# Performance work log

Hardware: AMD Instinct MI355X
Metric: run time of the kernel (lower is better)

## Reference

```python
import jax, jax.numpy as jnp
import numpy as np

N = 4096
DIN, DOUT, HID, CUTS = 16, 16, 16, 8
RADIUS = 9.0
SCALES = (1.0, 2.0, 3.0, 5.0, 10.0)
REG = 0.01
CHUNK = 512
GROUPS = 4
DINF = DIN + 2 * len(SCALES)  # 26


def leaky(v):
    return jnp.where(v >= 0, v, 0.2 * v)


def sqdist(a, b):
    d2 = jnp.sum(a * a, -1)[:, None] + jnp.sum(b * b, -1)[None, :] - 2.0 * (a @ b.T)
    return jnp.maximum(d2, 0.0)


def tangent_vectors(n):
    # Duff et al. branchless orthonormal basis, as in dMaSIF geometry_processing
    x, y, z = n[..., 0], n[..., 1], n[..., 2]
    s = jnp.where(z >= 0, 1.0, -1.0)
    a = -1.0 / (s + z)
    b = x * y * a
    t1 = jnp.stack([1.0 + s * x * x * a, s * b, -s * x], -1)
    t2 = jnp.stack([b, s + y * y * a, -y], -1)
    return jnp.stack([t1, t2], axis=-2)  # (..., 2, 3)


def group_norm(x, w, b, eps=1e-5):
    # torch GroupNorm(4, C) applied on (1, C, N): normalize over (C/G, N) per group
    n, c = x.shape
    xt = x.T.reshape(GROUPS, c // GROUPS, n)
    m = jnp.mean(xt, axis=(1, 2), keepdims=True)
    v = jnp.mean((xt - m) ** 2, axis=(1, 2), keepdims=True)
    xt = (xt - m) / jnp.sqrt(v + eps)
    return (xt.reshape(c, n) * w[:, None] + b[:, None]).T


def curvature_features(verts, normals):
    # dMaSIF curvatures(): per-scale Gaussian-window covariances, shape operator S = PPt^-1 PQt
    # Pairwise sums factorized into matmuls with the (N,N) window (no (N,N,8) intermediates).
    n_pts = verts.shape[0]
    d2 = sqdist(verts, verts)
    xx = (verts[:, :, None] * verts[:, None, :]).reshape(n_pts, 9)
    feats = []
    for s in SCALES:
        w = jnp.exp(-d2 / (2.0 * s * s))
        u_n = w @ normals  # scale-smoothed normals
        ns = u_n / jnp.maximum(jnp.linalg.norm(u_n, axis=-1, keepdims=True), 1e-12)
        uv = tangent_vectors(ns)  # (N,2,3)
        s0 = jnp.sum(w, 1)
        sx = w @ verts
        sn = w @ ns
        sxx = (w @ xx).reshape(n_pts, 3, 3)
        xn = (verts[:, :, None] * ns[:, None, :]).reshape(n_pts, 9)
        sxn = (w @ xn).reshape(n_pts, 3, 3)
        # sum_j w_ij (x_j-x_i)(x_j-x_i)^T  and  sum_j w_ij (x_j-x_i)(n_j-n_i)^T
        cxx = sxx - verts[:, :, None] * sx[:, None, :] - sx[:, :, None] * verts[:, None, :] \
              + s0[:, None, None] * verts[:, :, None] * verts[:, None, :]
        cxn = sxn - verts[:, :, None] * sn[:, None, :] - sx[:, :, None] * ns[:, None, :] \
              + s0[:, None, None] * verts[:, :, None] * ns[:, None, :]
        ppt = jnp.einsum('nka,nab,nlb->nkl', uv, cxx, uv) + REG * jnp.eye(2, dtype=verts.dtype)
        pqt = jnp.einsum('nka,nab,nlb->nkl', uv, cxn, uv)
        S = jnp.linalg.solve(ppt, pqt)  # (N,2,2)
        feats.append(jnp.clip(S[:, 0, 0] + S[:, 1, 1], -1.0, 1.0))            # mean curvature
        feats.append(jnp.clip(S[:, 0, 0] * S[:, 1, 1] - S[:, 0, 1] * S[:, 1, 0], -1.0, 1.0))  # gauss
    return jnp.stack(feats, -1)  # (N, 2*len(SCALES))


def _forward(verts, vnormals, x, os_w1, os_b1, os_w2, os_b2,
             ni_w1, ni_b1, ni_w2, ni_b2, gn_in_w, gn_in_b,
             cv_a1, cv_b1, cv_a2, cv_b2, no_w1, no_b1, no_w2, no_b2,
             gn_out_w, gn_out_b, ll_w1, ll_b1, ll_w2, ll_b2, lt_w, lt_b):
    curv = curvature_features(verts, vnormals)
    xf = jnp.concatenate([x, curv], axis=-1)  # (N, DINF)
    w = leaky(xf @ os_w1.T + os_b1) @ os_w2.T + os_b2  # orientation scores (N,1)

    # --- load_mesh: steer tangent frames along the gradient of w ---
    p = verts / RADIUS
    ndot = vnormals @ vnormals.T
    W = jnp.exp(-sqdist(p, p) * (2.0 - ndot) ** 2)  # pseudo-geodesic Gaussian window
    uv = tangent_vectors(vnormals)  # (N,2,3)
    ov3 = W @ (w * p) - (W @ w) * p  # sum_j W_ij w_j (x_j - x_i), factorized
    ov = jnp.einsum('nkd,nd->nk', uv, ov3) + 1e-5
    u = ov / jnp.sqrt(jnp.sum(ov * ov, -1, keepdims=True))
    ex, ey = u[:, 0:1], u[:, 1:2]
    u0, v0 = uv[:, 0], uv[:, 1]
    nuv = jnp.concatenate([vnormals[:, None, :],
                           (ex * u0 + ey * v0)[:, None, :],
                           (-ey * u0 + ex * v0)[:, None, :]], axis=1)  # (N,3,3)

    # --- dMaSIFConv layer ---
    h = leaky(leaky(xf @ ni_w1.T + ni_b1) @ ni_w2.T + ni_b2)
    h = group_norm(h, gn_in_w, gn_in_b)  # (N, HID)
    n_all = nuv[:, 0]
    nc = N // CHUNK
    pc = p.reshape(nc, CHUNK, 3)
    nuvc = nuv.reshape(nc, CHUNK, 3, 3)

    def block(args):
        pi, nuvi = args  # (C,3), (C,3,3)
        dx = p[None, :, :] - pi[:, None, :]  # (C,N,3)
        d2 = jnp.sum(dx * dx, -1)
        win = jnp.exp(-d2 * (2.0 - nuvi[:, 0] @ n_all.T) ** 2)  # (C,N)
        X = jnp.einsum('ckd,cnd->cnk', nuvi, dx)  # local coords (C,N,3)
        y = jax.nn.relu(X @ cv_a1.T + cv_b1) @ cv_a2.T + cv_b2  # filter MLP (C,N,HID)
        return jnp.einsum('cn,cnh,nh->ch', win, y, h)

    xi = jax.lax.map(jax.checkpoint(block), (pc, nuvc)).reshape(N, HID)
    xi = group_norm(leaky(leaky(xi @ no_w1.T + no_b1) @ no_w2.T + no_b2), gn_out_w, gn_out_b)
    xi = jax.nn.relu(xi @ ll_w1.T + ll_b1) @ ll_w2.T + ll_b2  # linear_layers[0]
    return xf @ lt_w.T + lt_b + xi  # linear_transform skip + conv branch


def setup_inputs():
    key = jax.random.key(0)
    ks = jax.random.split(key, 20)

    def lin(k, o, i):
        wk = jax.random.fold_in(k, 0)
        bk = jax.random.fold_in(k, 1)
        return ((1.0 / np.sqrt(i)) * jax.random.normal(wk, (o, i)),
                0.01 * jax.random.normal(bk, (o,)))

    verts = 10.0 * jax.random.normal(ks[0], (N, 3))
    vn = jax.random.normal(ks[1], (N, 3))
    vnormals = vn / jnp.linalg.norm(vn, axis=-1, keepdims=True)
    x = jax.random.normal(ks[2], (N, DIN))
    os_w1, os_b1 = lin(ks[3], DOUT, DINF)
    os_w2, os_b2 = lin(ks[4], 1, DOUT)
    ni_w1, ni_b1 = lin(ks[5], HID, DINF)
    ni_w2, ni_b2 = lin(ks[6], HID, HID)
    cv_a1 = jax.random.normal(ks[7], (CUTS, 3))
    cv_b1 = jax.random.uniform(ks[8], (CUTS,)) * 0.8 * jnp.sqrt(jnp.sum(cv_a1 ** 2, -1))
    cv_a2 = jax.random.uniform(ks[9], (HID, CUTS), minval=-1.0, maxval=1.0) / np.sqrt(CUTS)
    cv_b2 = jax.random.normal(ks[10], (HID,)) * 0.5 * jnp.sqrt(jnp.sum(cv_a2 ** 2, -1))
    no_w1, no_b1 = lin(ks[11], DOUT, HID)
    no_w2, no_b2 = lin(ks[12], DOUT, DOUT)
    ll_w1, ll_b1 = lin(ks[13], DOUT, DOUT)
    ll_w2, ll_b2 = lin(ks[14], DOUT, DOUT)
    lt_w, lt_b = lin(ks[15], DOUT, DINF)
    return {'verts': verts, 'vnormals': vnormals, 'x': x,
            'os_w1': os_w1, 'os_b1': os_b1, 'os_w2': os_w2, 'os_b2': os_b2,
            'ni_w1': ni_w1, 'ni_b1': ni_b1, 'ni_w2': ni_w2, 'ni_b2': ni_b2,
            'gn_in_w': jnp.ones(HID), 'gn_in_b': jnp.zeros(HID),
            'cv_a1': cv_a1, 'cv_b1': cv_b1, 'cv_a2': cv_a2, 'cv_b2': cv_b2,
            'no_w1': no_w1, 'no_b1': no_b1, 'no_w2': no_w2, 'no_b2': no_b2,
            'gn_out_w': jnp.ones(DOUT), 'gn_out_b': jnp.zeros(DOUT),
            'll_w1': ll_w1, 'll_b1': ll_b1, 'll_w2': ll_w2, 'll_b2': ll_b2,
            'lt_w': lt_w, 'lt_b': lt_b}


def reference(verts, vnormals, x, os_w1, os_b1, os_w2, os_b2,
              ni_w1, ni_b1, ni_w2, ni_b2, gn_in_w, gn_in_b,
              cv_a1, cv_b1, cv_a2, cv_b2, no_w1, no_b1, no_w2, no_b2,
              gn_out_w, gn_out_b, ll_w1, ll_b1, ll_w2, ll_b2, lt_w, lt_b):
    return _forward(verts, vnormals, x, os_w1, os_b1, os_w2, os_b2,
                    ni_w1, ni_b1, ni_w2, ni_b2, gn_in_w, gn_in_b,
                    cv_a1, cv_b1, cv_a2, cv_b2, no_w1, no_b1, no_w2, no_b2,
                    gn_out_w, gn_out_b, ll_w1, ll_b1, ll_w2, ll_b2, lt_w, lt_b)
```

## Files before the change

### kernel.cpp

```cpp
#include <hip/hip_runtime.h>
#include <hip/hip_bf16.h>
#include <math.h>

#define NPTS 4096
#define DINF 26
#define LOG2E 1.44269504088896f

typedef float f32x4v __attribute__((ext_vector_type(4)));
typedef __bf16 bf16x8v __attribute__((ext_vector_type(8)));

__device__ __forceinline__ float ldb(const float* p, int i){ return p[i]; }
__device__ __forceinline__ float lk(float v){ return v >= 0.0f ? v : 0.2f*v; }
__device__ __forceinline__ float wsum64(float v){
#pragma unroll
  for(int o=32;o>0;o>>=1) v += __shfl_down(v,o);
  return v;
}
__device__ __forceinline__ unsigned short f2bf(float f){
  return __builtin_bit_cast(unsigned short, __float2bfloat16(f));
}
__device__ __forceinline__ float bf2f(unsigned short u){
  return __bfloat162float(__builtin_bit_cast(__hip_bfloat16, u));
}
__device__ __forceinline__ unsigned pk2(float a, float b){
  return (unsigned)f2bf(a) | ((unsigned)f2bf(b)<<16);
}
__device__ __forceinline__ void split2(float a, float b, unsigned& h, unsigned& l){
  unsigned short ah=f2bf(a), bh=f2bf(b);
  float ar = a - bf2f(ah), br = b - bf2f(bh);
  h = (unsigned)ah | ((unsigned)bh<<16);
  l = (unsigned)f2bf(ar) | ((unsigned)f2bf(br)<<16);
}
__device__ __forceinline__ void wave_lds_fence(){
  __builtin_amdgcn_wave_barrier();
  __builtin_amdgcn_s_waitcnt(0xC07F);
  __builtin_amdgcn_wave_barrier();
}
__device__ __forceinline__ void tangent(float nx,float ny,float nz,float* t1,float* t2){
  float s = (nz >= 0.0f) ? 1.0f : -1.0f;
  float a = -1.0f/(s+nz);
  float b = nx*ny*a;
  t1[0]=1.0f+s*nx*nx*a; t1[1]=s*b; t1[2]=-s*nx;
  t2[0]=b; t2[1]=s+ny*ny*a; t2[2]=-ny;
}

__global__ __launch_bounds__(256) void k0_convert(const float* __restrict__ verts,
                                                  const float* __restrict__ vnorm,
                                                  const float* __restrict__ x,
                                                  float* __restrict__ vertsF,
                                                  float* __restrict__ nF,
                                                  float* __restrict__ pF,
                                                  float* __restrict__ xfF){
  int i = blockIdx.x*blockDim.x + threadIdx.x;
  if(i >= NPTS) return;
#pragma unroll
  for(int d=0;d<3;d++){
    float v = verts[i*3+d];
    vertsF[i*3+d]=v;
    pF[i*3+d]=v*(1.0f/9.0f);
    nF[i*3+d]=vnorm[i*3+d];
  }
#pragma unroll
  for(int c=0;c<16;c++) xfF[i*DINF+c]=x[i*16+c];
}

__global__ __launch_bounds__(512) void k1m(const float* __restrict__ vertsF,
                                           const float* __restrict__ nF,
                                           float* __restrict__ sc){
  __shared__ unsigned short fbh[8][64][18];
  __shared__ unsigned short fbl[8][64][18];
  __shared__ float vq[8][64][4];
  __shared__ float red[8][16][16];
  const float c2e[5] = {0.5f*LOG2E, 0.125f*LOG2E, (1.0f/18.0f)*LOG2E,
                        0.02f*LOG2E, 0.005f*LOG2E};
  int lane = threadIdx.x & 63, w = threadIdx.x >> 6;
  int c16 = lane & 15, q = lane >> 4;
  int i0 = blockIdx.x*16;
  int ia = i0 + c16;
  float vix=vertsF[ia*3+0], viy=vertsF[ia*3+1], viz=vertsF[ia*3+2];
  float nsqi = vix*vix+viy*viy+viz*viz;
  f32x4v acc[5];
#pragma unroll
  for(int s=0;s<5;s++) acc[s] = (f32x4v){0.0f,0.0f,0.0f,0.0f};

#pragma unroll 1
  for(int jb = w*512; jb < (w+1)*512; jb += 64){
    int j = jb + lane;
    float vx=vertsF[j*3+0], vy=vertsF[j*3+1], vz=vertsF[j*3+2];
    float nx=nF[j*3+0], ny=nF[j*3+1], nz=nF[j*3+2];
    float nsq = vx*vx+vy*vy+vz*vz;
    unsigned* fh = (unsigned*)&fbh[w][lane][0];
    unsigned* fl = (unsigned*)&fbl[w][lane][0];
    unsigned h,l;
    split2(1.0f, vx, h,l);      fh[0]=h; fl[0]=l;
    split2(vy, vz, h,l);        fh[1]=h; fl[1]=l;
    split2(vx*vx, vx*vy, h,l);  fh[2]=h; fl[2]=l;
    split2(vx*vz, vy*vy, h,l);  fh[3]=h; fl[3]=l;
    split2(vy*vz, vz*vz, h,l);  fh[4]=h; fl[4]=l;
    split2(nx, ny, h,l);        fh[5]=h; fl[5]=l;
    split2(nz, 0.0f, h,l);      fh[6]=h; fl[6]=l;
    fh[7]=0u; fl[7]=0u; fh[8]=0u; fl[8]=0u;
    *(float4*)&vq[w][lane][0] = make_float4(vx,vy,vz,nsq);
    wave_lds_fence();
#pragma unroll
    for(int q2=0;q2<2;q2++){
      int rb = q2*32 + q*8;
      bf16x8v bh, bl;
#pragma unroll
      for(int t=0;t<8;t++){
        bh[t] = __builtin_bit_cast(__bf16, fbh[w][rb+t][c16]);
        bl[t] = __builtin_bit_cast(__bf16, fbl[w][rb+t][c16]);
      }
      bf16x8v af[5];
#pragma unroll
      for(int t=0;t<8;t++){
        float4 vv = *(const float4*)&vq[w][rb+t][0];
        float dot = vix*vv.x + viy*vv.y + viz*vv.z;
        float d2 = fmaxf(nsqi + vv.w - 2.0f*dot, 0.0f);
#pragma unroll
        for(int s=0;s<5;s++)
          af[s][t] = __builtin_bit_cast(__bf16, f2bf(exp2f(-d2*c2e[s])));
      }
#pragma unroll
      for(int s=0;s<5;s++){
        acc[s] = __builtin_amdgcn_mfma_f32_16x16x32_bf16(af[s], bh, acc[s], 0,0,0);
        acc[s] = __builtin_amdgcn_mfma_f32_16x16x32_bf16(af[s], bl, acc[s], 0,0,0);
      }
    }
    wave_lds_fence();
  }
#pragma unroll
  for(int s=0;s<5;s++){
#pragma unroll
    for(int r=0;r<4;r++) red[w][q*4+r][c16] = acc[s][r];
    __syncthreads();
    if(w==0){
      float* base = sc + (size_t)s*13*NPTS;
#pragma unroll
      for(int r=0;r<4;r++){
        int m = q*4+r, i = i0+m;
        float D = 0.0f;
#pragma unroll
        for(int ww=0;ww<8;ww++) D += red[ww][m][c16];
        if(c16==0)       base[i]=D;
        else if(c16<4)   base[NPTS + i*3 + (c16-1)] = D;
        else if(c16<10)  base[4*NPTS + i*6 + (c16-4)] = D;
        else if(c16<13)  base[10*NPTS + i*3 + (c16-10)] = D;
      }
    }
    __syncthreads();
  }
}

__global__ __launch_bounds__(512) void k2m(const float* __restrict__ vertsF,
                                           float* __restrict__ sc,
                                           float* __restrict__ xfF){
  __shared__ unsigned short fbh[8][64][18];
  __shared__ unsigned short fbl[8][64][18];
  __shared__ float vq[8][64][4];
  __shared__ float red[8][16][16];
  const float c2e[5] = {0.5f*LOG2E, 0.125f*LOG2E, (1.0f/18.0f)*LOG2E,
                        0.02f*LOG2E, 0.005f*LOG2E};
  int lane = threadIdx.x & 63, w = threadIdx.x >> 6;
  int c16 = lane & 15, q = lane >> 4;
  int i0 = blockIdx.x*16;
  int ia = i0 + c16;
  float vix=vertsF[ia*3+0], viy=vertsF[ia*3+1], viz=vertsF[ia*3+2];
  float nsqi = vix*vix+viy*viy+viz*viz;
  f32x4v acc[5];
#pragma unroll
  for(int s=0;s<5;s++) acc[s] = (f32x4v){0.0f,0.0f,0.0f,0.0f};

#pragma unroll 1
  for(int jb = w*512; jb < (w+1)*512; jb += 64){
    int j = jb + lane;
    float vx=vertsF[j*3+0], vy=vertsF[j*3+1], vz=vertsF[j*3+2];
    float nsq = vx*vx+vy*vy+vz*vz;
    *(float4*)&vq[w][lane][0] = make_float4(vx,vy,vz,nsq);
    wave_lds_fence();
    float d2c[2][8];
#pragma unroll
    for(int q2=0;q2<2;q2++)
#pragma unroll
      for(int t=0;t<8;t++){
        float4 vv = *(const float4*)&vq[w][q2*32+q*8+t][0];
        float dot = vix*vv.x + viy*vv.y + viz*vv.z;
        d2c[q2][t] = fmaxf(nsqi + vv.w - 2.0f*dot, 0.0f);
      }
#pragma unroll
    for(int s=0;s<5;s++){
      const float* ub = sc + (size_t)s*13*NPTS + 10*NPTS + (size_t)j*3;
      float ux=ub[0], uy=ub[1], uz=ub[2];
      float inv = 1.0f/fmaxf(sqrtf(ux*ux+uy*uy+uz*uz), 1e-12f);
      float n0=ux*inv, n1=uy*inv, n2=uz*inv;
      unsigned* fh = (unsigned*)&fbh[w][lane][0];
      unsigned* fl = (unsigned*)&fbl[w][lane][0];
      unsigned h,l;
      split2(n0, n1, h,l);        fh[0]=h; fl[0]=l;
      split2(n2, vx*n0, h,l);     fh[1]=h; fl[1]=l;
      split2(vx*n1, vx*n2, h,l);  fh[2]=h; fl[2]=l;
      split2(vy*n0, vy*n1, h,l);  fh[3]=h; fl[3]=l;
      split2(vy*n2, vz*n0, h,l);  fh[4]=h; fl[4]=l;
      split2(vz*n1, vz*n2, h,l);  fh[5]=h; fl[5]=l;
      fh[6]=0u; fl[6]=0u; fh[7]=0u; fl[7]=0u; fh[8]=0u; fl[8]=0u;
      wave_lds_fence();
#pragma unroll
      for(int q2=0;q2<2;q2++){
        int rb = q2*32 + q*8;
        bf16x8v af, bh, bl;
#pragma unroll
        for(int t=0;t<8;t++){
          af[t] = __builtin_bit_cast(__bf16, f2bf(exp2f(-d2c[q2][t]*c2e[s])));
          bh[t] = __builtin_bit_cast(__bf16, fbh[w][rb+t][c16]);
          bl[t] = __builtin_bit_cast(__bf16, fbl[w][rb+t][c16]);
        }
        acc[s] = __builtin_amdgcn_mfma_f32_16x16x32_bf16(af, bh, acc[s], 0,0,0);
        acc[s] = __builtin_amdgcn_mfma_f32_16x16x32_bf16(af, bl, acc[s], 0,0,0);
      }
      wave_lds_fence();
    }
  }
#pragma unroll
  for(int s=0;s<5;s++){
#pragma unroll
    for(int r=0;r<4;r++) red[w][q*4+r][c16] = acc[s][r];
    __syncthreads();
    if(w==0){
#pragma unroll
      for(int r=0;r<4;r++){
        int m = q*4+r;
        float D = 0.0f;
#pragma unroll
        for(int ww=0;ww<8;ww++) D += red[ww][m][c16];
        red[0][m][c16] = D;
      }
    }
    __syncthreads();
    if(threadIdx.x < 16){
      int tid = threadIdx.x, i = i0 + tid;
      const float* base = sc + (size_t)s*13*NPTS;
      float v[3] = { vertsF[i*3+0], vertsF[i*3+1], vertsF[i*3+2] };
      float s0 = base[i];
      float sx[3] = { base[NPTS+i*3+0], base[NPTS+i*3+1], base[NPTS+i*3+2] };
      float sxx6[6];
#pragma unroll
      for(int k=0;k<6;k++) sxx6[k]=base[4*NPTS+i*6+k];
      float ux=base[10*NPTS+i*3+0], uy=base[10*NPTS+i*3+1], uz=base[10*NPTS+i*3+2];
      float invn = 1.0f/fmaxf(sqrtf(ux*ux+uy*uy+uz*uz), 1e-12f);
      float nsi[3] = { ux*invn, uy*invn, uz*invn };
      float sn[3] = { red[0][tid][0], red[0][tid][1], red[0][tid][2] };
      float sxn[3][3];
#pragma unroll
      for(int a=0;a<3;a++)
#pragma unroll
        for(int b=0;b<3;b++) sxn[a][b]=red[0][tid][3+a*3+b];
      const int m6[3][3]={{0,1,2},{1,3,4},{2,4,5}};
      float cxx[3][3], cxn[3][3];
#pragma unroll
      for(int a=0;a<3;a++)
#pragma unroll
        for(int b=0;b<3;b++){
          cxx[a][b]=sxx6[m6[a][b]] - v[a]*sx[b] - sx[a]*v[b] + s0*v[a]*v[b];
          cxn[a][b]=sxn[a][b]    - v[a]*sn[b] - sx[a]*nsi[b] + s0*v[a]*nsi[b];
        }
      float t1[3],t2[3];
      tangent(nsi[0],nsi[1],nsi[2],t1,t2);
      float ppt[2][2], pqt[2][2];
#pragma unroll
      for(int k=0;k<2;k++){
        const float* tk = (k==0)?t1:t2;
#pragma unroll
        for(int l=0;l<2;l++){
          const float* tl = (l==0)?t1:t2;
          float accx=0.0f, accn=0.0f;
#pragma unroll
          for(int a=0;a<3;a++)
#pragma unroll
            for(int b=0;b<3;b++){
              accx += tk[a]*cxx[a][b]*tl[b];
              accn += tk[a]*cxn[a][b]*tl[b];
            }
          ppt[k][l]=accx + ((k==l)?0.01f:0.0f);
          pqt[k][l]=accn;
        }
      }
      float det = ppt[0][0]*ppt[1][1]-ppt[0][1]*ppt[1][0];
      float id = 1.0f/det;
      float S00=( ppt[1][1]*pqt[0][0]-ppt[0][1]*pqt[1][0])*id;
      float S01=( ppt[1][1]*pqt[0][1]-ppt[0][1]*pqt[1][1])*id;
      float S10=(-ppt[1][0]*pqt[0][0]+ppt[0][0]*pqt[1][0])*id;
      float S11=(-ppt[1][0]*pqt[0][1]+ppt[0][0]*pqt[1][1])*id;
      float f0=fminf(fmaxf(S00+S11,-1.0f),1.0f);
      float f1=fminf(fmaxf(S00*S11-S01*S10,-1.0f),1.0f);
      xfF[i*DINF+16+2*s]=f0;
      xfF[i*DINF+17+2*s]=f1;
    }
    __syncthreads();
  }
}

__global__ __launch_bounds__(256) void k3_mlps(const float* __restrict__ xfF,
    const float* os_w1, const float* os_b1, const float* os_w2, const float* os_b2,
    const float* ni_w1, const float* ni_b1, const float* ni_w2, const float* ni_b2,
    float* __restrict__ wOS, float* __restrict__ hPre, float* __restrict__ stats){
  int i = blockIdx.x*256 + threadIdx.x;
  int lane = threadIdx.x & 63;
  float xf[DINF];
#pragma unroll
  for(int k=0;k<DINF;k++) xf[k]=xfF[i*DINF+k];
  float h1[16];
#pragma unroll
  for(int o=0;o<16;o++){
    float t=ldb(os_b1,o);
#pragma unroll
    for(int k=0;k<DINF;k++) t += xf[k]*ldb(os_w1,o*DINF+k);
    h1[o]=lk(t);
  }
  float w=ldb(os_b2,0);
#pragma unroll
  for(int o=0;o<16;o++) w += h1[o]*ldb(os_w2,o);
  wOS[i]=w;
#pragma unroll
  for(int o=0;o<16;o++){
    float t=ldb(ni_b1,o);
#pragma unroll
    for(int k=0;k<DINF;k++) t += xf[k]*ldb(ni_w1,o*DINF+k);
    h1[o]=lk(t);
  }
  float h2[16];
#pragma unroll
  for(int o=0;o<16;o++){
    float t=ldb(ni_b2,o);
#pragma unroll
    for(int k=0;k<16;k++) t += h1[k]*ldb(ni_w2,o*16+k);
    h2[o]=lk(t);
    hPre[i*16+o]=h2[o];
  }
  float gs[4]={0,0,0,0}, gq[4]={0,0,0,0};
#pragma unroll
  for(int c=0;c<16;c++){ gs[c>>2]+=h2[c]; gq[c>>2]+=h2[c]*h2[c]; }
  __shared__ float ls[8];
  if(threadIdx.x<8) ls[threadIdx.x]=0.0f;
  __syncthreads();
#pragma unroll
  for(int g=0;g<4;g++){ gs[g]=wsum64(gs[g]); gq[g]=wsum64(gq[g]); }
  if(lane==0){
#pragma unroll
    for(int g=0;g<4;g++){ atomicAdd(&ls[2*g],gs[g]); atomicAdd(&ls[2*g+1],gq[g]); }
  }
  __syncthreads();
  if(threadIdx.x<8) atomicAdd(&stats[threadIdx.x], ls[threadIdx.x]);
}

__global__ __launch_bounds__(256) void k3c_gn(const float* __restrict__ hPre,
                                              const float* __restrict__ stats,
                                              const float* gw, const float* gb,
                                              unsigned short* __restrict__ hTb){
  int i = blockIdx.x*256 + threadIdx.x;
  float m[4], r[4];
#pragma unroll
  for(int g=0;g<4;g++){
    float mean = stats[2*g]*(1.0f/(4.0f*NPTS));
    float var  = stats[2*g+1]*(1.0f/(4.0f*NPTS)) - mean*mean;
    m[g]=mean; r[g]=1.0f/sqrtf(var+1e-5f);
  }
#pragma unroll
  for(int c=0;c<16;c++){
    int g=c>>2;
    float v=(hPre[i*16+c]-m[g])*r[g]*ldb(gw,c)+ldb(gb,c);
    hTb[c*NPTS+i]=f2bf(v);
  }
}

__global__ __launch_bounds__(256) void k4_ov(const float* __restrict__ pF,
                                             const float* __restrict__ nF,
                                             const float* __restrict__ wOS,
                                             float* __restrict__ nuvF){
  int lane = threadIdx.x & 63;
  int i = blockIdx.x*4 + (threadIdx.x>>6);
  float pix=pF[i*3+0], piy=pF[i*3+1], piz=pF[i*3+2];
  float nix=nF[i*3+0], niy=nF[i*3+1], niz=nF[i*3+2];
  float a0=0,a1=0,a2=0,a3=0;
#pragma unroll 1
  for(int j=lane;j<NPTS;j+=64){
    float px=pF[j*3+0], py=pF[j*3+1], pz=pF[j*3+2];
    float nx=nF[j*3+0], ny=nF[j*3+1], nz=nF[j*3+2];
    float wj=wOS[j];
    float dx=px-pix, dy=py-piy, dz=pz-piz;
    float d2=dx*dx+dy*dy+dz*dz;
    float f=2.0f-(nx*nix+ny*niy+nz*niz);
    float Wv=__expf(-d2*f*f);
    float Ww=Wv*wj;
    a0+=Ww*px; a1+=Ww*py; a2+=Ww*pz; a3+=Ww;
  }
  a0=wsum64(a0); a1=wsum64(a1); a2=wsum64(a2); a3=wsum64(a3);
  if(lane==0){
    float o0=a0-a3*pix, o1=a1-a3*piy, o2=a2-a3*piz;
    float t1[3],t2[3];
    tangent(nix,niy,niz,t1,t2);
    float ov0=t1[0]*o0+t1[1]*o1+t1[2]*o2+1e-5f;
    float ov1=t2[0]*o0+t2[1]*o1+t2[2]*o2+1e-5f;
    float inv=1.0f/sqrtf(ov0*ov0+ov1*ov1);
    float ex=ov0*inv, ey=ov1*inv;
    nuvF[i*9+0]=nix; nuvF[i*9+1]=niy; nuvF[i*9+2]=niz;
    nuvF[i*9+3]= ex*t1[0]+ey*t2[0]; nuvF[i*9+4]= ex*t1[1]+ey*t2[1]; nuvF[i*9+5]= ex*t1[2]+ey*t2[2];
    nuvF[i*9+6]=-ey*t1[0]+ex*t2[0]; nuvF[i*9+7]=-ey*t1[1]+ex*t2[1]; nuvF[i*9+8]=-ey*t1[2]+ex*t2[2];
  }
}

__global__ __launch_bounds__(256) void k5_conv(const float* __restrict__ pF,
                                               const float* __restrict__ nF,
                                               const float* __restrict__ nuvF,
                                               const unsigned short* __restrict__ hTb,
                                               const float* cv_a1, const float* cv_b1,
                                               const float* cv_a2, const float* cv_b2,
                                               float* __restrict__ xiF){
  __shared__ unsigned short zs[4][64][18];
  int lane = threadIdx.x & 63;
  int w = threadIdx.x >> 6;
  int i = blockIdx.x*4 + w;
  int c16 = lane & 15, q = lane >> 4;
  unsigned* zr = (unsigned*)&zs[w][lane][0];
#pragma unroll
  for(int c=0;c<9;c++) zr[c]=0u;

  float pix=pF[i*3+0], piy=pF[i*3+1], piz=pF[i*3+2];
  float nu[9];
#pragma unroll
  for(int k=0;k<9;k++) nu[k]=nuvF[i*9+k];
  float a1w[8][3], b1w[8];
#pragma unroll
  for(int c=0;c<8;c++){
    a1w[c][0]=cv_a1[c*3+0]; a1w[c][1]=cv_a1[c*3+1]; a1w[c][2]=cv_a1[c*3+2];
    b1w[c]=cv_b1[c];
  }
  const unsigned short* hrow = hTb + c16*NPTS;
  f32x4v acc = {0.0f,0.0f,0.0f,0.0f};
  wave_lds_fence();

#pragma unroll 1
  for(int jb=0; jb<NPTS; jb+=64){
    int j = jb + lane;
    float px=pF[j*3+0], py=pF[j*3+1], pz=pF[j*3+2];
    float nx=nF[j*3+0], ny=nF[j*3+1], nz=nF[j*3+2];
    float dx=px-pix, dy=py-piy, dz=pz-piz;
    float d2=dx*dx+dy*dy+dz*dz;
    float f=2.0f-(nx*nu[0]+ny*nu[1]+nz*nu[2]);
    float win=__expf(-d2*f*f);
    float X0=nu[0]*dx+nu[1]*dy+nu[2]*dz;
    float X1=nu[3]*dx+nu[4]*dy+nu[5]*dz;
    float X2=nu[6]*dx+nu[7]*dy+nu[8]*dz;
    float z[8];
#pragma unroll
    for(int c=0;c<8;c++){
      float r=fmaf(X0,a1w[c][0],fmaf(X1,a1w[c][1],fmaf(X2,a1w[c][2],b1w[c])));
      z[c]=win*fmaxf(r,0.0f);
    }
    zr[0]=pk2(z[0],z[1]); zr[1]=pk2(z[2],z[3]);
    zr[2]=pk2(z[4],z[5]); zr[3]=pk2(z[6],z[7]);
    zr[4]=(unsigned)f2bf(win);
    wave_lds_fence();
#pragma unroll
    for(int q2=0;q2<2;q2++){
      int jb2 = jb + q2*32;
      bf16x8v afr = *(const bf16x8v*)(hrow + jb2 + q*8);
      bf16x8v bfr;
#pragma unroll
      for(int t=0;t<8;t++)
        bfr[t] = __builtin_bit_cast(__bf16, zs[w][q2*32 + q*8 + t][c16]);
      acc = __builtin_amdgcn_mfma_f32_16x16x32_bf16(afr, bfr, acc, 0, 0, 0);
    }
    wave_lds_fence();
  }
#pragma unroll
  for(int r=0;r<4;r++){
    int h = q*4 + r;
    float coef = (c16<8) ? cv_a2[h*8+c16] : ((c16==8) ? cv_b2[h] : 0.0f);
    float v = acc[r]*coef;
#pragma unroll
    for(int o=1;o<16;o<<=1) v += __shfl_xor(v,o);
    if(c16==0) xiF[i*16+h]=v;
  }
}

__global__ __launch_bounds__(256) void k6a(const float* __restrict__ xiF,
    const float* no_w1, const float* no_b1, const float* no_w2, const float* no_b2,
    float* __restrict__ tF, float* __restrict__ stats2){
  int i = blockIdx.x*256 + threadIdx.x;
  int lane = threadIdx.x & 63;
  float xi[16];
#pragma unroll
  for(int k=0;k<16;k++) xi[k]=xiF[i*16+k];
  float t1[16];
#pragma unroll
  for(int o=0;o<16;o++){
    float t=ldb(no_b1,o);
#pragma unroll
    for(int k=0;k<16;k++) t += xi[k]*ldb(no_w1,o*16+k);
    t1[o]=lk(t);
  }
  float t2[16];
#pragma unroll
  for(int o=0;o<16;o++){
    float t=ldb(no_b2,o);
#pragma unroll
    for(int k=0;k<16;k++) t += t1[k]*ldb(no_w2,o*16+k);
    t2[o]=lk(t);
    tF[i*16+o]=t2[o];
  }
  float gs[4]={0,0,0,0}, gq[4]={0,0,0,0};
#pragma unroll
  for(int c=0;c<16;c++){ gs[c>>2]+=t2[c]; gq[c>>2]+=t2[c]*t2[c]; }
  __shared__ float ls[8];
  if(threadIdx.x<8) ls[threadIdx.x]=0.0f;
  __syncthreads();
#pragma unroll
  for(int g=0;g<4;g++){ gs[g]=wsum64(gs[g]); gq[g]=wsum64(gq[g]); }
  if(lane==0){
#pragma unroll
    for(int g=0;g<4;g++){ atomicAdd(&ls[2*g],gs[g]); atomicAdd(&ls[2*g+1],gq[g]); }
  }
  __syncthreads();
  if(threadIdx.x<8) atomicAdd(&stats2[threadIdx.x], ls[threadIdx.x]);
}

__global__ __launch_bounds__(256) void k6c(const float* __restrict__ tF,
    const float* __restrict__ xfF, const float* __restrict__ stats2,
    const float* gw, const float* gb,
    const float* ll_w1, const float* ll_b1, const float* ll_w2, const float* ll_b2,
    const float* lt_w, const float* lt_b,
    float* __restrict__ out){
  int i = blockIdx.x*256 + threadIdx.x;
  float m[4], r[4];
#pragma unroll
  for(int g=0;g<4;g++){
    float mean = stats2[2*g]*(1.0f/(4.0f*NPTS));
    float var  = stats2[2*g+1]*(1.0f/(4.0f*NPTS)) - mean*mean;
    m[g]=mean; r[g]=1.0f/sqrtf(var+1e-5f);
  }
  float tn[16];
#pragma unroll
  for(int c=0;c<16;c++){
    int g=c>>2;
    tn[c]=(tF[i*16+c]-m[g])*r[g]*ldb(gw,c)+ldb(gb,c);
  }
  float z1[16];
#pragma unroll
  for(int o=0;o<16;o++){
    float t=ldb(ll_b1,o);
#pragma unroll
    for(int k=0;k<16;k++) t += tn[k]*ldb(ll_w1,o*16+k);
    z1[o]=fmaxf(t,0.0f);
  }
  float xf[DINF];
#pragma unroll
  for(int k=0;k<DINF;k++) xf[k]=xfF[i*DINF+k];
#pragma unroll
  for(int o=0;o<16;o++){
    float z=ldb(ll_b2,o);
#pragma unroll
    for(int k=0;k<16;k++) z += z1[k]*ldb(ll_w2,o*16+k);
    float lt=ldb(lt_b,o);
#pragma unroll
    for(int k=0;k<DINF;k++) lt += xf[k]*ldb(lt_w,o*DINF+k);
    out[i*16+o]=z+lt;
  }
}

extern "C" void kernel_launch(void* const* d_in, const int* in_sizes, int n_in,
                              void* d_out, int out_size, void* d_ws, size_t ws_size,
                              hipStream_t stream){
  const float* verts    = (const float*)d_in[0];
  const float* vnormals = (const float*)d_in[1];
  const float* x        = (const float*)d_in[2];
  const float* os_w1    = (const float*)d_in[3];
  const float* os_b1    = (const float*)d_in[4];
  const float* os_w2    = (const float*)d_in[5];
  const float* os_b2    = (const float*)d_in[6];
  const float* ni_w1    = (const float*)d_in[7];
  const float* ni_b1    = (const float*)d_in[8];
  const float* ni_w2    = (const float*)d_in[9];
  const float* ni_b2    = (const float*)d_in[10];
  const float* gn_in_w  = (const float*)d_in[11];
  const float* gn_in_b  = (const float*)d_in[12];
  const float* cv_a1    = (const float*)d_in[13];
  const float* cv_b1    = (const float*)d_in[14];
  const float* cv_a2    = (const float*)d_in[15];
  const float* cv_b2    = (const float*)d_in[16];
  const float* no_w1    = (const float*)d_in[17];
  const float* no_b1    = (const float*)d_in[18];
  const float* no_w2    = (const float*)d_in[19];
  const float* no_b2    = (const float*)d_in[20];
  const float* gn_out_w = (const float*)d_in[21];
  const float* gn_out_b = (const float*)d_in[22];
  const float* ll_w1    = (const float*)d_in[23];
  const float* ll_b1    = (const float*)d_in[24];
  const float* ll_w2    = (const float*)d_in[25];
  const float* ll_b2    = (const float*)d_in[26];
  const float* lt_w     = (const float*)d_in[27];
  const float* lt_b     = (const float*)d_in[28];

  float* W = (float*)d_ws;
  size_t off = 0;
  float* vertsF = W + off; off += (size_t)3*NPTS;
  float* nF     = W + off; off += (size_t)3*NPTS;
  float* pF     = W + off; off += (size_t)3*NPTS;
  float* xfF    = W + off; off += (size_t)DINF*NPTS;
  float* sc     = W + off; off += (size_t)13*NPTS*5;
  float* wOS    = W + off; off += (size_t)NPTS;
  float* hPre   = W + off; off += (size_t)16*NPTS;
  unsigned short* hTb = (unsigned short*)(W + off); off += (size_t)8*NPTS;
  float* nuvF   = W + off; off += (size_t)9*NPTS;
  float* xiF    = W + off; off += (size_t)16*NPTS;
  float* tF     = W + off; off += (size_t)16*NPTS;
  float* stats  = W + off; off += 16;

  hipMemsetAsync(stats, 0, 16*sizeof(float), stream);

  k0_convert<<<NPTS/256, 256, 0, stream>>>(verts, vnormals, x, vertsF, nF, pF, xfF);
  k1m<<<NPTS/16, 512, 0, stream>>>(vertsF, nF, sc);
  k2m<<<NPTS/16, 512, 0, stream>>>(vertsF, sc, xfF);
  k3_mlps<<<NPTS/256, 256, 0, stream>>>(xfF, os_w1, os_b1, os_w2, os_b2,
                                        ni_w1, ni_b1, ni_w2, ni_b2, wOS, hPre, stats);
  k3c_gn<<<NPTS/256, 256, 0, stream>>>(hPre, stats, gn_in_w, gn_in_b, hTb);
  k4_ov<<<NPTS/4, 256, 0, stream>>>(pF, nF, wOS, nuvF);
  k5_conv<<<NPTS/4, 256, 0, stream>>>(pF, nF, nuvF, hTb, cv_a1, cv_b1, cv_a2, cv_b2, xiF);
  k6a<<<NPTS/256, 256, 0, stream>>>(xiF, no_w1, no_b1, no_w2, no_b2, tF, stats+8);
  k6c<<<NPTS/256, 256, 0, stream>>>(tF, xfF, stats+8, gn_out_w, gn_out_b,
                                    ll_w1, ll_b1, ll_w2, ll_b2, lt_w, lt_b, (float*)d_out);
}
```

Measured before the change: 343.1 us.

## Split j-range across blocks/waves in pairwise kernels to raise parallelism

The two curvature moment kernels now launch twice as many blocks, each covering half of the j range, and combine partial sums with atomicAdd into zeroed buffers. The per-point shape-operator finalisation moves into a new elementwise kernel k2s. k4_ov and k5_conv split each row's j loop across two waves and merge the halves through shared memory. The aim is more blocks on a 4096-point problem so more CUs stay busy, at the cost of atomics, extra memsets, another launch, and float results that are no longer deterministic.

```diff
diff --git a/kernel.cpp b/kernel.cpp
--- a/kernel.cpp
+++ b/kernel.cpp
@@ -75,7 +75,8 @@
                         0.02f*LOG2E, 0.005f*LOG2E};
   int lane = threadIdx.x & 63, w = threadIdx.x >> 6;
   int c16 = lane & 15, q = lane >> 4;
-  int i0 = blockIdx.x*16;
+  int it = blockIdx.x >> 1, jh = blockIdx.x & 1;
+  int i0 = it*16;
   int ia = i0 + c16;
   float vix=vertsF[ia*3+0], viy=vertsF[ia*3+1], viz=vertsF[ia*3+2];
   float nsqi = vix*vix+viy*viy+viz*viz;
@@ -83,8 +84,9 @@
 #pragma unroll
   for(int s=0;s<5;s++) acc[s] = (f32x4v){0.0f,0.0f,0.0f,0.0f};
 
+  int jbeg = jh*2048 + w*256;
 #pragma unroll 1
-  for(int jb = w*512; jb < (w+1)*512; jb += 64){
+  for(int jb = jbeg; jb < jbeg+256; jb += 64){
     int j = jb + lane;
     float vx=vertsF[j*3+0], vy=vertsF[j*3+1], vz=vertsF[j*3+2];
     float nx=nF[j*3+0], ny=nF[j*3+1], nz=nF[j*3+2];
@@ -142,10 +144,10 @@
         float D = 0.0f;
 #pragma unroll
         for(int ww=0;ww<8;ww++) D += red[ww][m][c16];
-        if(c16==0)       base[i]=D;
-        else if(c16<4)   base[NPTS + i*3 + (c16-1)] = D;
-        else if(c16<10)  base[4*NPTS + i*6 + (c16-4)] = D;
-        else if(c16<13)  base[10*NPTS + i*3 + (c16-10)] = D;
+        if(c16==0)       atomicAdd(&base[i], D);
+        else if(c16<4)   atomicAdd(&base[NPTS + i*3 + (c16-1)], D);
+        else if(c16<10)  atomicAdd(&base[4*NPTS + i*6 + (c16-4)], D);
+        else if(c16<13)  atomicAdd(&base[10*NPTS + i*3 + (c16-10)], D);
       }
     }
     __syncthreads();
@@ -153,8 +155,8 @@
 }
 
 __global__ __launch_bounds__(512) void k2m(const float* __restrict__ vertsF,
-                                           float* __restrict__ sc,
-                                           float* __restrict__ xfF){
+                                           const float* __restrict__ sc,
+                                           float* __restrict__ mom2){
   __shared__ unsigned short fbh[8][64][18];
   __shared__ unsigned short fbl[8][64][18];
   __shared__ float vq[8][64][4];
@@ -163,7 +165,8 @@
                         0.02f*LOG2E, 0.005f*LOG2E};
   int lane = threadIdx.x & 63, w = threadIdx.x >> 6;
   int c16 = lane & 15, q = lane >> 4;
-  int i0 = blockIdx.x*16;
+  int it = blockIdx.x >> 1, jh = blockIdx.x & 1;
+  int i0 = it*16;
   int ia = i0 + c16;
   float vix=vertsF[ia*3+0], viy=vertsF[ia*3+1], viz=vertsF[ia*3+2];
   float nsqi = vix*vix+viy*viy+viz*viz;
@@ -171,8 +174,9 @@
 #pragma unroll
   for(int s=0;s<5;s++) acc[s] = (f32x4v){0.0f,0.0f,0.0f,0.0f};
 
+  int jbeg = jh*2048 + w*256;
 #pragma unroll 1
-  for(int jb = w*512; jb < (w+1)*512; jb += 64){
+  for(int jb = jbeg; jb < jbeg+256; jb += 64){
     int j = jb + lane;
     float vx=vertsF[j*3+0], vy=vertsF[j*3+1], vz=vertsF[j*3+2];
     float nsq = vx*vx+vy*vy+vz*vz;
@@ -228,75 +232,81 @@
     if(w==0){
 #pragma unroll
       for(int r=0;r<4;r++){
-        int m = q*4+r;
+        int m = q*4+r, i = i0+m;
         float D = 0.0f;
 #pragma unroll
         for(int ww=0;ww<8;ww++) D += red[ww][m][c16];
-        red[0][m][c16] = D;
+        if(c16<12) atomicAdd(&mom2[((size_t)s*NPTS + i)*12 + c16], D);
       }
     }
     __syncthreads();
-    if(threadIdx.x < 16){
-      int tid = threadIdx.x, i = i0 + tid;
-      const float* base = sc + (size_t)s*13*NPTS;
-      float v[3] = { vertsF[i*3+0], vertsF[i*3+1], vertsF[i*3+2] };
-      float s0 = base[i];
-      float sx[3] = { base[NPTS+i*3+0], base[NPTS+i*3+1], base[NPTS+i*3+2] };
-      float sxx6[6];
-#pragma unroll
-      for(int k=0;k<6;k++) sxx6[k]=base[4*NPTS+i*6+k];
-      float ux=base[10*NPTS+i*3+0], uy=base[10*NPTS+i*3+1], uz=base[10*NPTS+i*3+2];
-      float invn = 1.0f/fmaxf(sqrtf(ux*ux+uy*uy+uz*uz), 1e-12f);
-      float nsi[3] = { ux*invn, uy*invn, uz*invn };
-      float sn[3] = { red[0][tid][0], red[0][tid][1], red[0][tid][2] };
-      float sxn[3][3];
+  }
+}
+
+__global__ __launch_bounds__(256) void k2s(const float* __restrict__ vertsF,
+                                           const float* __restrict__ sc,
+                                           const float* __restrict__ mom2,
+                                           float* __restrict__ xfF){
+  int idx = blockIdx.x*256 + threadIdx.x;
+  int i = idx & (NPTS-1);
+  int s = idx >> 12;
+  const float* base = sc + (size_t)s*13*NPTS;
+  float v[3] = { vertsF[i*3+0], vertsF[i*3+1], vertsF[i*3+2] };
+  float s0 = base[i];
+  float sx[3] = { base[NPTS+i*3+0], base[NPTS+i*3+1], base[NPTS+i*3+2] };
+  float sxx6[6];
+#pragma unroll
+  for(int k=0;k<6;k++) sxx6[k]=base[4*NPTS+i*6+k];
+  float ux=base[10*NPTS+i*3+0], uy=base[10*NPTS+i*3+1], uz=base[10*NPTS+i*3+2];
+  float invn = 1.0f/fmaxf(sqrtf(ux*ux+uy*uy+uz*uz), 1e-12f);
+  float nsi[3] = { ux*invn, uy*invn, uz*invn };
+  const float* M2 = mom2 + ((size_t)s*NPTS + i)*12;
+  float sn[3] = { M2[0], M2[1], M2[2] };
+  float sxn[3][3];
+#pragma unroll
+  for(int a=0;a<3;a++)
+#pragma unroll
+    for(int b=0;b<3;b++) sxn[a][b]=M2[3+a*3+b];
+  const int m6[3][3]={{0,1,2},{1,3,4},{2,4,5}};
+  float cxx[3][3], cxn[3][3];
+#pragma unroll
+  for(int a=0;a<3;a++)
+#pragma unroll
+    for(int b=0;b<3;b++){
+      cxx[a][b]=sxx6[m6[a][b]] - v[a]*sx[b] - sx[a]*v[b] + s0*v[a]*v[b];
+      cxn[a][b]=sxn[a][b]    - v[a]*sn[b] - sx[a]*nsi[b] + s0*v[a]*nsi[b];
+    }
+  float t1[3],t2[3];
+  tangent(nsi[0],nsi[1],nsi[2],t1,t2);
+  float ppt[2][2], pqt[2][2];
+#pragma unroll
+  for(int k=0;k<2;k++){
+    const float* tk = (k==0)?t1:t2;
+#pragma unroll
+    for(int l=0;l<2;l++){
+      const float* tl = (l==0)?t1:t2;
+      float accx=0.0f, accn=0.0f;
 #pragma unroll
       for(int a=0;a<3;a++)
 #pragma unroll
-        for(int b=0;b<3;b++) sxn[a][b]=red[0][tid][3+a*3+b];
-      const int m6[3][3]={{0,1,2},{1,3,4},{2,4,5}};
-      float cxx[3][3], cxn[3][3];
-#pragma unroll
-      for(int a=0;a<3;a++)
-#pragma unroll
         for(int b=0;b<3;b++){
-          cxx[a][b]=sxx6[m6[a][b]] - v[a]*sx[b] - sx[a]*v[b] + s0*v[a]*v[b];
-          cxn[a][b]=sxn[a][b]    - v[a]*sn[b] - sx[a]*nsi[b] + s0*v[a]*nsi[b];
+          accx += tk[a]*cxx[a][b]*tl[b];
+          accn += tk[a]*cxn[a][b]*tl[b];
         }
-      float t1[3],t2[3];
-      tangent(nsi[0],nsi[1],nsi[2],t1,t2);
-      float ppt[2][2], pqt[2][2];
-#pragma unroll
-      for(int k=0;k<2;k++){
-        const float* tk = (k==0)?t1:t2;
-#pragma unroll
-        for(int l=0;l<2;l++){
-          const float* tl = (l==0)?t1:t2;
-          float accx=0.0f, accn=0.0f;
-#pragma unroll
-          for(int a=0;a<3;a++)
-#pragma unroll
-            for(int b=0;b<3;b++){
-              accx += tk[a]*cxx[a][b]*tl[b];
-              accn += tk[a]*cxn[a][b]*tl[b];
-            }
-          ppt[k][l]=accx + ((k==l)?0.01f:0.0f);
-          pqt[k][l]=accn;
-        }
-      }
-      float det = ppt[0][0]*ppt[1][1]-ppt[0][1]*ppt[1][0];
-      float id = 1.0f/det;
-      float S00=( ppt[1][1]*pqt[0][0]-ppt[0][1]*pqt[1][0])*id;
-      float S01=( ppt[1][1]*pqt[0][1]-ppt[0][1]*pqt[1][1])*id;
-      float S10=(-ppt[1][0]*pqt[0][0]+ppt[0][0]*pqt[1][0])*id;
-      float S11=(-ppt[1][0]*pqt[0][1]+ppt[0][0]*pqt[1][1])*id;
-      float f0=fminf(fmaxf(S00+S11,-1.0f),1.0f);
-      float f1=fminf(fmaxf(S00*S11-S01*S10,-1.0f),1.0f);
-      xfF[i*DINF+16+2*s]=f0;
-      xfF[i*DINF+17+2*s]=f1;
-    }
-    __syncthreads();
-  }
+      ppt[k][l]=accx + ((k==l)?0.01f:0.0f);
+      pqt[k][l]=accn;
+    }
+  }
+  float det = ppt[0][0]*ppt[1][1]-ppt[0][1]*ppt[1][0];
+  float id = 1.0f/det;
+  float S00=( ppt[1][1]*pqt[0][0]-ppt[0][1]*pqt[1][0])*id;
+  float S01=( ppt[1][1]*pqt[0][1]-ppt[0][1]*pqt[1][1])*id;
+  float S10=(-ppt[1][0]*pqt[0][0]+ppt[0][0]*pqt[1][0])*id;
+  float S11=(-ppt[1][0]*pqt[0][1]+ppt[0][0]*pqt[1][1])*id;
+  float f0=fminf(fmaxf(S00+S11,-1.0f),1.0f);
+  float f1=fminf(fmaxf(S00*S11-S01*S10,-1.0f),1.0f);
+  xfF[i*DINF+16+2*s]=f0;
+  xfF[i*DINF+17+2*s]=f1;
 }
 
 __global__ __launch_bounds__(256) void k3_mlps(const float* __restrict__ xfF,
@@ -376,13 +386,16 @@
                                              const float* __restrict__ nF,
                                              const float* __restrict__ wOS,
                                              float* __restrict__ nuvF){
+  __shared__ float part[4][4];
   int lane = threadIdx.x & 63;
-  int i = blockIdx.x*4 + (threadIdx.x>>6);
+  int w = threadIdx.x >> 6;
+  int ii = w >> 1, jh = w & 1;
+  int i = blockIdx.x*2 + ii;
   float pix=pF[i*3+0], piy=pF[i*3+1], piz=pF[i*3+2];
   float nix=nF[i*3+0], niy=nF[i*3+1], niz=nF[i*3+2];
   float a0=0,a1=0,a2=0,a3=0;
 #pragma unroll 1
-  for(int j=lane;j<NPTS;j+=64){
+  for(int j=jh*2048+lane; j<jh*2048+2048; j+=64){
     float px=pF[j*3+0], py=pF[j*3+1], pz=pF[j*3+2];
     float nx=nF[j*3+0], ny=nF[j*3+1], nz=nF[j*3+2];
     float wj=wOS[j];
@@ -394,7 +407,11 @@
     a0+=Ww*px; a1+=Ww*py; a2+=Ww*pz; a3+=Ww;
   }
   a0=wsum64(a0); a1=wsum64(a1); a2=wsum64(a2); a3=wsum64(a3);
-  if(lane==0){
+  if(lane==0){ part[w][0]=a0; part[w][1]=a1; part[w][2]=a2; part[w][3]=a3; }
+  __syncthreads();
+  if(lane==0 && jh==0){
+    a0=part[w][0]+part[w+1][0]; a1=part[w][1]+part[w+1][1];
+    a2=part[w][2]+part[w+1][2]; a3=part[w][3]+part[w+1][3];
     float o0=a0-a3*pix, o1=a1-a3*piy, o2=a2-a3*piz;
     float t1[3],t2[3];
     tangent(nix,niy,niz,t1,t2);
@@ -416,9 +433,11 @@
                                                const float* cv_a2, const float* cv_b2,
                                                float* __restrict__ xiF){
   __shared__ unsigned short zs[4][64][18];
+  __shared__ float red[4][64][4];
   int lane = threadIdx.x & 63;
   int w = threadIdx.x >> 6;
-  int i = blockIdx.x*4 + w;
+  int ii = w >> 1, jh = w & 1;
+  int i = blockIdx.x*2 + ii;
   int c16 = lane & 15, q = lane >> 4;
   unsigned* zr = (unsigned*)&zs[w][lane][0];
 #pragma unroll
@@ -439,7 +458,7 @@
   wave_lds_fence();
 
 #pragma unroll 1
-  for(int jb=0; jb<NPTS; jb+=64){
+  for(int jb=jh*2048; jb<jh*2048+2048; jb+=64){
     int j = jb + lane;
     float px=pF[j*3+0], py=pF[j*3+1], pz=pF[j*3+2];
     float nx=nF[j*3+0], ny=nF[j*3+1], nz=nF[j*3+2];
@@ -473,13 +492,18 @@
     wave_lds_fence();
   }
 #pragma unroll
-  for(int r=0;r<4;r++){
-    int h = q*4 + r;
-    float coef = (c16<8) ? cv_a2[h*8+c16] : ((c16==8) ? cv_b2[h] : 0.0f);
-    float v = acc[r]*coef;
-#pragma unroll
-    for(int o=1;o<16;o<<=1) v += __shfl_xor(v,o);
-    if(c16==0) xiF[i*16+h]=v;
+  for(int r=0;r<4;r++) red[w][lane][r]=acc[r];
+  __syncthreads();
+  if(jh==0){
+#pragma unroll
+    for(int r=0;r<4;r++){
+      int h = q*4 + r;
+      float coef = (c16<8) ? cv_a2[h*8+c16] : ((c16==8) ? cv_b2[h] : 0.0f);
+      float v = (red[w][lane][r]+red[w+1][lane][r])*coef;
+#pragma unroll
+      for(int o=1;o<16;o<<=1) v += __shfl_xor(v,o);
+      if(c16==0) xiF[i*16+h]=v;
+    }
   }
 }
 
@@ -614,17 +638,21 @@
   float* xiF    = W + off; off += (size_t)16*NPTS;
   float* tF     = W + off; off += (size_t)16*NPTS;
   float* stats  = W + off; off += 16;
+  float* mom2 = hPre;
 
   hipMemsetAsync(stats, 0, 16*sizeof(float), stream);
+  hipMemsetAsync(sc,   0, (size_t)13*NPTS*5*sizeof(float), stream);
+  hipMemsetAsync(mom2, 0, (size_t)12*NPTS*5*sizeof(float), stream);
 
   k0_convert<<<NPTS/256, 256, 0, stream>>>(verts, vnormals, x, vertsF, nF, pF, xfF);
-  k1m<<<NPTS/16, 512, 0, stream>>>(vertsF, nF, sc);
-  k2m<<<NPTS/16, 512, 0, stream>>>(vertsF, sc, xfF);
+  k1m<<<NPTS/8, 512, 0, stream>>>(vertsF, nF, sc);
+  k2m<<<NPTS/8, 512, 0, stream>>>(vertsF, sc, mom2);
+  k2s<<<5*NPTS/256, 256, 0, stream>>>(vertsF, sc, mom2, xfF);
   k3_mlps<<<NPTS/256, 256, 0, stream>>>(xfF, os_w1, os_b1, os_w2, os_b2,
                                         ni_w1, ni_b1, ni_w2, ni_b2, wOS, hPre, stats);
   k3c_gn<<<NPTS/256, 256, 0, stream>>>(hPre, stats, gn_in_w, gn_in_b, hTb);
-  k4_ov<<<NPTS/4, 256, 0, stream>>>(pF, nF, wOS, nuvF);
-  k5_conv<<<NPTS/4, 256, 0, stream>>>(pF, nF, nuvF, hTb, cv_a1, cv_b1, cv_a2, cv_b2, xiF);
+  k4_ov<<<NPTS/2, 256, 0, stream>>>(pF, nF, wOS, nuvF);
+  k5_conv<<<NPTS/2, 256, 0, stream>>>(pF, nF, nuvF, hTb, cv_a1, cv_b1, cv_a2, cv_b2, xiF);
   k6a<<<NPTS/256, 256, 0, stream>>>(xiF, no_w1, no_b1, no_w2, no_b2, tF, stats+8);
   k6c<<<NPTS/256, 256, 0, stream>>>(tF, xfF, stats+8, gn_out_w, gn_out_b,
                                     ll_w1, ll_b1, ll_w2, ll_b2, lt_w, lt_b, (float*)d_out);
```

Result: no change. 344.5 us (+0.4%).
